# Kernel tuning notes

Measured on AMD Instinct MI355X. Metric: run time of the kernel, lower is better.

The kernel has to match this reference:

```python
import jax, jax.numpy as jnp
import numpy as np

N = 32768        # atoms
INV = 256        # irreps_in[inv_field].dim (scalar latent width)
MUL = 32         # input eq multiplicity: '32x1o'
VOUT = 4         # output eq multiplicity: '4x1o'
HID = 512        # ScalarMLPFunction latent dims [512, 512]
INV_OUT = 2      # inv_out_irreps '2x0e'
TYPES = 32       # num_types
EPS = 1e-10


def _mlp(x, w1, w2, w3):
    # ScalarMLPFunction: Linear(+1/sqrt(fan_in) norm) -> SiLU -> ... -> Linear
    h = jax.nn.silu((x @ w1) * (1.0 / np.sqrt(w1.shape[0])))
    h = jax.nn.silu((h @ w2) * (1.0 / np.sqrt(w2.shape[0])))
    return (h @ w3) * (1.0 / np.sqrt(w3.shape[0]))


def setup_inputs() -> dict:
    key = jax.random.key(0)
    ks = jax.random.split(key, 10)
    inv_features = jax.random.normal(ks[0], (N, INV), dtype=jnp.float32)
    eq_features = jax.random.normal(ks[1], (N, MUL, 3), dtype=jnp.float32)
    atom_types = jax.random.randint(ks[2], (N, 1), 0, TYPES, dtype=jnp.int32)
    # hypernetwork (final_latent): INV -> 512 -> 512 -> MUL*VOUT
    w1_lat = jax.random.normal(ks[3], (INV, HID), dtype=jnp.float32)
    w2_lat = jax.random.normal(ks[4], (HID, HID), dtype=jnp.float32)
    w3_lat = jax.random.normal(ks[5], (HID, MUL * VOUT), dtype=jnp.float32)
    # final_readout: INV -> 512 -> 512 -> INV_OUT
    w1_ro = jax.random.normal(ks[6], (INV, HID), dtype=jnp.float32)
    w2_ro = jax.random.normal(ks[7], (HID, HID), dtype=jnp.float32)
    w3_ro = jax.random.normal(ks[8], (HID, INV_OUT), dtype=jnp.float32)
    # atom_type2bond_lengths parameter, init to ones as in the module
    bond_lengths = jnp.ones((TYPES, VOUT, 1), dtype=jnp.float32)
    return dict(inv_features=inv_features, eq_features=eq_features,
                atom_types=atom_types, w1_lat=w1_lat, w2_lat=w2_lat,
                w3_lat=w3_lat, w1_ro=w1_ro, w2_ro=w2_ro, w3_ro=w3_ro,
                bond_lengths=bond_lengths)


def reference(inv_features, eq_features, atom_types, w1_lat, w2_lat, w3_lat,
              w1_ro, w2_ro, w3_ro, bond_lengths):
    # hypernet-generated per-atom weights for the equivariant Linear
    weights = _mlp(inv_features, w1_lat, w2_lat, w3_lat)          # [N, MUL*VOUT]
    weights = weights.reshape(-1, MUL, VOUT)                      # [N, u, v]
    inv_out = _mlp(inv_features, w1_ro, w2_ro, w3_ro)             # [N, INV_OUT]
    # e3nn Linear '32x1o -> 4x1o', shared_weights=False, path norm 1/sqrt(mul_in)
    eq = jnp.einsum('num,nuv->nvm', eq_features, weights) * (1.0 / np.sqrt(MUL))
    # norm -> divide -> nan_to_num
    norm = jnp.linalg.norm(eq, axis=-1, keepdims=True)            # [N, VOUT, 1]
    eq = jnp.nan_to_num(eq / (norm + EPS), nan=0.0)
    # per-atom-type bond-length scale (gather-multiply)
    eq = eq * bond_lengths[atom_types[:, 0]]                      # [N, VOUT, 3]
    return inv_out, eq
```

## Files before the change

kernel.cpp:

```cpp
#include <hip/hip_runtime.h>
#include <hip/hip_bf16.h>

#define N_ATOMS 32768

typedef __attribute__((ext_vector_type(4))) float f32x4;
typedef __attribute__((ext_vector_type(8))) short bf16x8;
typedef unsigned short u16;

__device__ __forceinline__ u16 f2b(float f) {
    union { __hip_bfloat16 b; u16 u; } c;
    c.b = __float2bfloat16(f);
    return c.u;
}
__device__ __forceinline__ float b2f(u16 u) {
    union { unsigned int i; float f; } c;
    c.i = ((unsigned int)u) << 16;
    return c.f;
}

#define GLDS16(src, dst) __builtin_amdgcn_global_load_lds( \
    (const __attribute__((address_space(1))) void*)(src),  \
    (__attribute__((address_space(3))) void*)(dst), 16, 0, 0)

__global__ void __launch_bounds__(256) setup_kernel(
        const float* __restrict__ x, u16* __restrict__ xhi, u16* __restrict__ xlo,
        const float* __restrict__ w1l, const float* __restrict__ w2l,
        const float* __restrict__ w3l, const float* __restrict__ w1r,
        const float* __restrict__ w2r,
        u16* __restrict__ W1LThi, u16* __restrict__ W1LTlo, u16* __restrict__ W1RT,
        u16* __restrict__ W2LThi, u16* __restrict__ W2LTlo, u16* __restrict__ W2RT,
        u16* __restrict__ W3LThi, u16* __restrict__ W3LTlo,
        float* __restrict__ out_inv) {
    int bid = blockIdx.x;
    if (bid < 4096) {
        size_t i = (size_t)(bid * 256 + threadIdx.x) * 8;
        float4 v0 = *(const float4*)(x + i);
        float4 v1 = *(const float4*)(x + i + 4);
        float v[8] = {v0.x, v0.y, v0.z, v0.w, v1.x, v1.y, v1.z, v1.w};
        bf16x8 rh, rl;
#pragma unroll
        for (int j = 0; j < 8; ++j) {
            u16 h = f2b(v[j]);
            rh[j] = (short)h;
            rl[j] = (short)f2b(v[j] - b2f(h));
        }
        *(bf16x8*)(xhi + i) = rh;
        *(bf16x8*)(xlo + i) = rl;
    } else if (bid < 7424) {
        int i = (bid - 4096) * 256 + threadIdx.x;
        if (i < 131072) {
            int n = i >> 8, k = i & 255;
            float v = w1l[k * 512 + n];
            u16 h = f2b(v);
            W1LThi[i] = h;
            W1LTlo[i] = f2b(v - b2f(h));
        } else if (i < 262144) {
            int j = i - 131072;
            int n = j >> 8, k = j & 255;
            W1RT[j] = f2b(w1r[k * 512 + n]);
        } else if (i < 524288) {
            int j = i - 262144;
            int n = j >> 9, k = j & 511;
            float v = w2l[k * 512 + n];
            u16 h = f2b(v);
            W2LThi[j] = h;
            W2LTlo[j] = f2b(v - b2f(h));
        } else if (i < 786432) {
            int j = i - 524288;
            int n = j >> 9, k = j & 511;
            W2RT[j] = f2b(w2r[k * 512 + n]);
        } else if (i < 851968) {
            int j = i - 786432;
            int n = j >> 9, k = j & 511;
            float v = w3l[k * 128 + n];
            u16 h = f2b(v);
            W3LThi[j] = h;
            W3LTlo[j] = f2b(v - b2f(h));
        }
    } else {
        int i = (bid - 7424) * 256 + threadIdx.x;
        *(float4*)(out_inv + i * 4) = float4{0.f, 0.f, 0.f, 0.f};
    }
}

template<int GX>
__global__ void __launch_bounds__(512, 1) gemm4p(
        const u16* __restrict__ Ahi, const u16* __restrict__ Alo,
        const u16* __restrict__ Bhi, const u16* __restrict__ Blo,
        u16* __restrict__ Chi, u16* __restrict__ Clo,
        int ldc, int K, float scale) {
    __shared__ __align__(16) u16 smem[65536];
    u16* const lA0 = smem;
    u16* const lB0 = smem + 32768;
    const int tid = threadIdx.x;
    const int lane = tid & 63;
    const int wid = tid >> 6;
    const int wm = wid >> 2;
    const int wn = wid & 3;
    const int rlane = lane & 15;
    const int kc = lane >> 4;
    const int srow0 = tid >> 2;
    const int scp = tid & 3;

    const int nwg = gridDim.x;
    const int bid = blockIdx.x;
    const int wg = (bid & 7) * (nwg >> 3) + (bid >> 3);
    const int bn = (wg % GX) * 256;
    const int bm = (wg / GX) * 256;

    const int kt = K >> 6;
    const int NT = 3 * kt;

    auto stageA = [&](int t, int buf, int kh) {
        int seg = (t >= kt) + (t >= 2 * kt);
        const u16* As = (seg == 1) ? Alo : Ahi;
        int k0 = (t - seg * kt) * 64 + kh * 32;
        u16* la = lA0 + buf * 16384 + kh * 8192;
#pragma unroll
        for (int call = 0; call < 2; ++call) {
            int row = call * 128 + srow0;
            int c = scp ^ ((row >> 1) & 3);
            GLDS16(As + (size_t)(bm + row) * K + k0 + c * 8, la + row * 32 + scp * 8);
        }
    };
    auto stageB = [&](int t, int buf, int kh) {
        int seg = (t >= kt) + (t >= 2 * kt);
        const u16* Bs = (seg == 2) ? Blo : Bhi;
        int k0 = (t - seg * kt) * 64 + kh * 32;
        u16* lb = lB0 + buf * 16384 + kh * 8192;
#pragma unroll
        for (int call = 0; call < 2; ++call) {
            int row = call * 128 + srow0;
            int c = scp ^ ((row >> 1) & 3);
            GLDS16(Bs + (size_t)(bn + row) * K + k0 + c * 8, lb + row * 32 + scp * 8);
        }
    };

    f32x4 acc[8][4] = {};
    bf16x8 af[4], bf[4];

#define RD_A(buf, kh, mh) do {                                                \
        const u16* la_ = lA0 + (buf) * 16384 + (kh) * 8192;                   \
        _Pragma("unroll")                                                     \
        for (int m_ = 0; m_ < 4; ++m_) {                                      \
            int row_ = wm * 128 + (mh) * 64 + m_ * 16 + rlane;                \
            int c_ = kc ^ ((row_ >> 1) & 3);                                  \
            af[m_] = *(const bf16x8*)&la_[row_ * 32 + c_ * 8];                \
        }                                                                     \
    } while (0)
#define RD_B(buf, kh) do {                                                    \
        const u16* lb_ = lB0 + (buf) * 16384 + (kh) * 8192;                   \
        _Pragma("unroll")                                                     \
        for (int n_ = 0; n_ < 4; ++n_) {                                      \
            int row_ = wn * 64 + n_ * 16 + rlane;                             \
            int c_ = kc ^ ((row_ >> 1) & 3);                                  \
            bf[n_] = *(const bf16x8*)&lb_[row_ * 32 + c_ * 8];                \
        }                                                                     \
    } while (0)
#define LGKM0 do {                                                            \
        asm volatile("s_waitcnt lgkmcnt(0)" ::: "memory");                    \
        __builtin_amdgcn_sched_barrier(0);                                    \
    } while (0)
#define MM(mh) do {                                                           \
        __builtin_amdgcn_s_setprio(1);                                        \
        _Pragma("unroll")                                                     \
        for (int m_ = 0; m_ < 4; ++m_)                                        \
            _Pragma("unroll")                                                 \
            for (int n_ = 0; n_ < 4; ++n_)                                    \
                acc[(mh) * 4 + m_][n_] = __builtin_amdgcn_mfma_f32_16x16x32_bf16( \
                    af[m_], bf[n_], acc[(mh) * 4 + m_][n_], 0, 0, 0);         \
        __builtin_amdgcn_s_setprio(0);                                        \
    } while (0)

    stageA(0, 0, 0);
    stageB(0, 0, 0);
    stageA(0, 0, 1);
    stageB(0, 0, 1);

    for (int t = 0; t < NT; ++t) {
        const int cur = t & 1, oth = cur ^ 1;
        const bool pf = (t + 1 < NT);
        asm volatile("s_waitcnt vmcnt(4)" ::: "memory");
        __builtin_amdgcn_s_barrier();
        RD_B(cur, 0);
        RD_A(cur, 0, 0);
        if (pf) stageA(t + 1, oth, 0);
        LGKM0;
        MM(0);
        RD_A(cur, 0, 1);
        if (pf) stageB(t + 1, oth, 0);
        LGKM0;
        MM(1);
        if (pf) asm volatile("s_waitcnt vmcnt(4)" ::: "memory");
        else    asm volatile("s_waitcnt vmcnt(0)" ::: "memory");
        __builtin_amdgcn_s_barrier();
        RD_B(cur, 1);
        RD_A(cur, 1, 0);
        if (pf) stageA(t + 1, oth, 1);
        LGKM0;
        MM(0);
        RD_A(cur, 1, 1);
        if (pf) stageB(t + 1, oth, 1);
        LGKM0;
        MM(1);
    }
#undef MM
#undef LGKM0
#undef RD_B
#undef RD_A

    const int g = lane >> 4;
#pragma unroll
    for (int m = 0; m < 8; ++m) {
        int grow0 = bm + wm * 128 + m * 16 + (g << 2);
#pragma unroll
        for (int n = 0; n < 4; ++n) {
            int gcol = bn + wn * 64 + n * 16 + rlane;
#pragma unroll
            for (int r = 0; r < 4; ++r) {
                float v = acc[m][n][r] * scale;
                v = v / (1.0f + __expf(-v));
                size_t idx = (size_t)(grow0 + r) * ldc + gcol;
                u16 h = f2b(v);
                Chi[idx] = h;
                Clo[idx] = f2b(v - b2f(h));
            }
        }
    }
}

template<int NSEG, int GX, int NF, bool SILU, int OUTK>
__global__ void __launch_bounds__(512, 2) gemm8p(
        const u16* __restrict__ Ahi, const u16* __restrict__ Alo,
        const u16* __restrict__ Bhi, const u16* __restrict__ Blo,
        void* __restrict__ Chi, void* __restrict__ Clo,
        int ldc, int K, float scale,
        const float* __restrict__ e_w3, float* __restrict__ e_out) {
    constexpr int LBSZ = NF * 64 * 64;
    constexpr int SMEMN = 32768 + 2 * LBSZ;
    __shared__ __align__(16) u16 smem[SMEMN];
    u16* const lA0 = smem;
    u16* const lB0 = smem + 32768;
    const int tid = threadIdx.x;
    const int lane = tid & 63;
    const int wid = tid >> 6;
    const int wm = wid >> 2;
    const int wn = wid & 3;
    const int rlane = lane & 15;
    const int kc = lane >> 4;
    const int cps = rlane & 7;
    const int srow = tid >> 3;
    const int scp = tid & 7;

    const int nwg = gridDim.x;
    const int bid = blockIdx.x;
    const int wg = (bid & 7) * (nwg >> 3) + (bid >> 3);
    const int bn = (wg % GX) * (NF * 64);
    const int bm = (wg / GX) * 256;

    const int kt = K >> 6;
    const int NT = NSEG * kt;

    auto stageA = [&](int t, int buf) {
        int seg = (NSEG == 1) ? 0 : ((t >= kt) + (t >= 2 * kt));
        const u16* As = (NSEG == 1) ? Ahi : (seg == 1 ? Alo : Ahi);
        int k0 = (t - seg * kt) << 6;
        u16* la = lA0 + buf * 16384;
#pragma unroll
        for (int call = 0; call < 4; ++call) {
            int row = call * 64 + srow;
            int c = scp ^ (row & 7);
            GLDS16(As + (size_t)(bm + row) * K + k0 + c * 8, la + (size_t)(row * 64 + scp * 8));
        }
    };
    auto stageB = [&](int t, int buf) {
        int seg = (NSEG == 1) ? 0 : ((t >= kt) + (t >= 2 * kt));
        const u16* Bs = (NSEG == 1) ? Bhi : (seg == 2 ? Blo : Bhi);
        int k0 = (t - seg * kt) << 6;
        u16* lb = lB0 + buf * LBSZ;
#pragma unroll
        for (int call = 0; call < NF; ++call) {
            int row = call * 64 + srow;
            int c = scp ^ (row & 7);
            GLDS16(Bs + (size_t)(bn + row) * K + k0 + c * 8, lb + (size_t)(row * 64 + scp * 8));
        }
    };

    f32x4 acc[8][NF] = {};

    stageA(0, 0);
    stageB(0, 0);
    asm volatile("s_waitcnt vmcnt(0)" ::: "memory");
    __builtin_amdgcn_s_barrier();

    for (int t = 0; t < NT; ++t) {
        const int cur = t & 1, nxt = cur ^ 1;
        const bool pf = (t + 1 < NT);
        const u16* la = lA0 + cur * 16384;
        const u16* lb = lB0 + cur * LBSZ;
#pragma unroll
        for (int ks = 0; ks < 2; ++ks) {
            bf16x8 af[8], bfr[NF];
            const int cp = (ks * 4 + kc) ^ cps;
#pragma unroll
            for (int m = 0; m < 8; ++m) {
                int row = wm * 128 + m * 16 + rlane;
                af[m] = *(const bf16x8*)&la[row * 64 + cp * 8];
            }
#pragma unroll
            for (int n = 0; n < NF; ++n) {
                int row = wn * (NF * 16) + n * 16 + rlane;
                bfr[n] = *(const bf16x8*)&lb[row * 64 + cp * 8];
            }
            if (pf) {
                if (ks == 0) stageA(t + 1, nxt);
                else         stageB(t + 1, nxt);
            }
            asm volatile("s_waitcnt lgkmcnt(0)" ::: "memory");
            __builtin_amdgcn_sched_barrier(0);
            __builtin_amdgcn_s_setprio(1);
#pragma unroll
            for (int m = 0; m < 8; ++m)
#pragma unroll
                for (int n = 0; n < NF; ++n)
                    acc[m][n] = __builtin_amdgcn_mfma_f32_16x16x32_bf16(af[m], bfr[n], acc[m][n], 0, 0, 0);
            __builtin_amdgcn_s_setprio(0);
        }
        asm volatile("s_waitcnt vmcnt(0)" ::: "memory");
        __builtin_amdgcn_s_barrier();
    }

    const int g = lane >> 4;

    if constexpr (OUTK == 3) {
        const float s512f = 0.04419417382415922f;
        float wj0[NF], wj1[NF];
#pragma unroll
        for (int n = 0; n < NF; ++n) {
            int gc = bn + wn * (NF * 16) + n * 16 + rlane;
            wj0[n] = e_w3[gc * 2] * s512f;
            wj1[n] = e_w3[gc * 2 + 1] * s512f;
        }
#pragma unroll
        for (int m = 0; m < 8; ++m)
#pragma unroll
            for (int r = 0; r < 4; ++r) {
                float s0 = 0.f, s1 = 0.f;
#pragma unroll
                for (int n = 0; n < NF; ++n) {
                    float v = acc[m][n][r] * scale;
                    v = v / (1.0f + __expf(-v));
                    s0 = fmaf(v, wj0[n], s0);
                    s1 = fmaf(v, wj1[n], s1);
                }
#pragma unroll
                for (int off = 1; off < 16; off <<= 1) {
                    s0 += __shfl_xor(s0, off);
                    s1 += __shfl_xor(s1, off);
                }
                if (rlane == 0) {
                    int row = bm + wm * 128 + m * 16 + g * 4 + r;
                    atomicAdd(&e_out[row * 2], s0);
                    atomicAdd(&e_out[row * 2 + 1], s1);
                }
            }
    } else {
#pragma unroll
        for (int m = 0; m < 8; ++m) {
            int grow0 = bm + wm * 128 + m * 16 + (g << 2);
#pragma unroll
            for (int n = 0; n < NF; ++n) {
                int gcol = bn + wn * (NF * 16) + n * 16 + rlane;
#pragma unroll
                for (int r = 0; r < 4; ++r) {
                    float v = acc[m][n][r] * scale;
                    if constexpr (SILU) v = v / (1.0f + __expf(-v));
                    size_t idx = (size_t)(grow0 + r) * ldc + gcol;
                    if constexpr (OUTK == 0) ((float*)Chi)[idx] = v;
                    else                     ((u16*)Chi)[idx] = f2b(v);
                }
            }
        }
    }
}

__global__ void eq_kernel(const float* __restrict__ eqf, const float* __restrict__ wgt,
                          const int* __restrict__ types, const float* __restrict__ bond,
                          float* __restrict__ out) {
    int t = blockIdx.x * 256 + threadIdx.x;
    int n = t >> 2, v = t & 3;
    const float* e = eqf + (size_t)n * 96;
    const float* w = wgt + (size_t)n * 128 + v;
    float a0 = 0.f, a1 = 0.f, a2 = 0.f;
#pragma unroll
    for (int u = 0; u < 32; ++u) {
        float wv = w[u * 4];
        a0 = fmaf(e[u * 3 + 0], wv, a0);
        a1 = fmaf(e[u * 3 + 1], wv, a1);
        a2 = fmaf(e[u * 3 + 2], wv, a2);
    }
    const float s = 0.17677669529663687f;
    a0 *= s; a1 *= s; a2 *= s;
    float norm = sqrtf(a0 * a0 + a1 * a1 + a2 * a2) + 1e-10f;
    float bl = bond[types[n] * 4 + v];
    float r0 = a0 / norm, r1 = a1 / norm, r2 = a2 / norm;
    if (isnan(r0)) r0 = 0.f;
    if (isnan(r1)) r1 = 0.f;
    if (isnan(r2)) r2 = 0.f;
    out[(size_t)n * 12 + v * 3 + 0] = r0 * bl;
    out[(size_t)n * 12 + v * 3 + 1] = r1 * bl;
    out[(size_t)n * 12 + v * 3 + 2] = r2 * bl;
}

extern "C" void kernel_launch(void* const* d_in, const int* in_sizes, int n_in,
                              void* d_out, int out_size, void* d_ws, size_t ws_size,
                              hipStream_t stream) {
    const float* inv  = (const float*)d_in[0];
    const float* eqf  = (const float*)d_in[1];
    const int*   typs = (const int*)d_in[2];
    const float* w1l  = (const float*)d_in[3];
    const float* w2l  = (const float*)d_in[4];
    const float* w3l  = (const float*)d_in[5];
    const float* w1r  = (const float*)d_in[6];
    const float* w2r  = (const float*)d_in[7];
    const float* w3r  = (const float*)d_in[8];
    const float* bond = (const float*)d_in[9];

    char* ws = (char*)d_ws;
    const size_t MB = 1024 * 1024, KB = 1024;
    u16* XHI   = (u16*)(ws);
    u16* XLO   = (u16*)(ws + 16 * MB);
    u16* H1R   = (u16*)(ws + 32 * MB);
    u16* H1Lhi = (u16*)(ws + 64 * MB);
    u16* H1Llo = (u16*)(ws + 96 * MB);
    u16* H2Lhi = (u16*)(ws);
    u16* H2Llo = (u16*)(ws + 128 * MB);
    float* WGT = (float*)(ws + 32 * MB);
    char* wb = ws + 160 * MB;
    u16* W1LThi = (u16*)(wb);
    u16* W1LTlo = (u16*)(wb + 256 * KB);
    u16* W1RT   = (u16*)(wb + 512 * KB);
    u16* W2LThi = (u16*)(wb + 768 * KB);
    u16* W2LTlo = (u16*)(wb + 1280 * KB);
    u16* W2RT   = (u16*)(wb + 1792 * KB);
    u16* W3LThi = (u16*)(wb + 2304 * KB);
    u16* W3LTlo = (u16*)(wb + 2432 * KB);

    float* out_inv = (float*)d_out;
    float* out_eq  = (float*)d_out + N_ATOMS * 2;

    const float s256 = 0.0625f;
    const float s512 = 0.04419417382415922f;

    setup_kernel<<<dim3(7488), dim3(256), 0, stream>>>(
        inv, XHI, XLO, w1l, w2l, w3l, w1r, w2r,
        W1LThi, W1LTlo, W1RT, W2LThi, W2LTlo, W2RT, W3LThi, W3LTlo, out_inv);
    gemm4p<2><<<dim3(256), dim3(512), 0, stream>>>(
        XHI, XLO, W1LThi, W1LTlo, H1Lhi, H1Llo, 512, 256, s256);
    gemm8p<1, 2, 4, true, 1><<<dim3(256), dim3(512), 0, stream>>>(
        XHI, nullptr, W1RT, nullptr, H1R, nullptr, 512, 256, s256, nullptr, nullptr);
    gemm8p<1, 2, 4, true, 3><<<dim3(256), dim3(512), 0, stream>>>(
        H1R, nullptr, W2RT, nullptr, nullptr, nullptr, 0, 512, s512, w3r, out_inv);
    gemm4p<2><<<dim3(256), dim3(512), 0, stream>>>(
        H1Lhi, H1Llo, W2LThi, W2LTlo, H2Lhi, H2Llo, 512, 512, s512);
    gemm8p<3, 2, 1, false, 0><<<dim3(256), dim3(512), 0, stream>>>(
        H2Lhi, H2Llo, W3LThi, W3LTlo, WGT, nullptr, 128, 512, s512, nullptr, nullptr);
    eq_kernel<<<dim3(512), dim3(256), 0, stream>>>(eqf, WGT, typs, bond, out_eq);
}
```

Before: 196.4 us.

## Restructure split-bf16 GEMM into 8-wave ping-pong with 64-wide K tiles

Replaces the 4-phase gemm4p with gemm8x, used for the first two latent MLP layers. The LDS layout changes from two 32-wide K halves per tile to row-halves with 64-wide K rows and an 8-way XOR swizzle. The main loop becomes a barrier-separated ping-pong schedule where each wave group alternates MFMA bursts with LDS reads and global-to-LDS prefetch. The aim is better overlap of MFMA with memory traffic and fewer LDS bank conflicts, at the cost of many more barriers and a full vmcnt(0) drain every iteration.

```diff
diff --git a/kernel.cpp b/kernel.cpp
--- a/kernel.cpp
+++ b/kernel.cpp
@@ -84,23 +84,24 @@
 }
 
 template<int GX>
-__global__ void __launch_bounds__(512, 1) gemm4p(
+__global__ void __launch_bounds__(512, 1) gemm8x(
         const u16* __restrict__ Ahi, const u16* __restrict__ Alo,
         const u16* __restrict__ Bhi, const u16* __restrict__ Blo,
         u16* __restrict__ Chi, u16* __restrict__ Clo,
         int ldc, int K, float scale) {
     __shared__ __align__(16) u16 smem[65536];
-    u16* const lA0 = smem;
-    u16* const lB0 = smem + 32768;
     const int tid = threadIdx.x;
     const int lane = tid & 63;
     const int wid = tid >> 6;
     const int wm = wid >> 2;
     const int wn = wid & 3;
+    const int bh = wn >> 1;
+    const int br0 = (wn & 1) * 64;
     const int rlane = lane & 15;
     const int kc = lane >> 4;
-    const int srow0 = tid >> 2;
-    const int scp = tid & 3;
+    const int cps = rlane & 7;
+    const int srow = tid >> 3;
+    const int scp = tid & 7;
 
     const int nwg = gridDim.x;
     const int bid = blockIdx.x;
@@ -111,103 +112,81 @@
     const int kt = K >> 6;
     const int NT = 3 * kt;
 
-    auto stageA = [&](int t, int buf, int kh) {
+    auto stage = [&](int t, int mat, int h) {
         int seg = (t >= kt) + (t >= 2 * kt);
-        const u16* As = (seg == 1) ? Alo : Ahi;
-        int k0 = (t - seg * kt) * 64 + kh * 32;
-        u16* la = lA0 + buf * 16384 + kh * 8192;
+        int k0 = (t - seg * kt) << 6;
+        int buf = t & 1;
+        const u16* src = (mat == 0) ? ((seg == 1) ? Alo : Ahi)
+                                    : ((seg == 2) ? Blo : Bhi);
+        int grow = ((mat == 0) ? bm : bn) + h * 128;
+        u16* dst = smem + mat * 32768 + buf * 16384 + h * 8192;
 #pragma unroll
         for (int call = 0; call < 2; ++call) {
-            int row = call * 128 + srow0;
-            int c = scp ^ ((row >> 1) & 3);
-            GLDS16(As + (size_t)(bm + row) * K + k0 + c * 8, la + row * 32 + scp * 8);
-        }
-    };
-    auto stageB = [&](int t, int buf, int kh) {
-        int seg = (t >= kt) + (t >= 2 * kt);
-        const u16* Bs = (seg == 2) ? Blo : Bhi;
-        int k0 = (t - seg * kt) * 64 + kh * 32;
-        u16* lb = lB0 + buf * 16384 + kh * 8192;
-#pragma unroll
-        for (int call = 0; call < 2; ++call) {
-            int row = call * 128 + srow0;
-            int c = scp ^ ((row >> 1) & 3);
-            GLDS16(Bs + (size_t)(bn + row) * K + k0 + c * 8, lb + row * 32 + scp * 8);
+            int row = call * 64 + srow;
+            int c = scp ^ (row & 7);
+            GLDS16(src + (size_t)(grow + row) * K + k0 + c * 8, dst + row * 64 + scp * 8);
         }
     };
 
     f32x4 acc[8][4] = {};
     bf16x8 af[4], bf[4];
 
-#define RD_A(buf, kh, mh) do {                                                \
-        const u16* la_ = lA0 + (buf) * 16384 + (kh) * 8192;                   \
-        _Pragma("unroll")                                                     \
-        for (int m_ = 0; m_ < 4; ++m_) {                                      \
-            int row_ = wm * 128 + (mh) * 64 + m_ * 16 + rlane;                \
-            int c_ = kc ^ ((row_ >> 1) & 3);                                  \
-            af[m_] = *(const bf16x8*)&la_[row_ * 32 + c_ * 8];                \
-        }                                                                     \
+#define RD_B(buf, kk) do {                                                     \
+        const u16* lb_ = smem + 32768 + (buf) * 16384 + bh * 8192;             \
+        _Pragma("unroll")                                                      \
+        for (int n_ = 0; n_ < 4; ++n_) {                                       \
+            int row_ = br0 + n_ * 16 + rlane;                                  \
+            bf[n_] = *(const bf16x8*)&lb_[row_ * 64 + (((kk) * 4 + kc) ^ cps) * 8]; \
+        }                                                                      \
     } while (0)
-#define RD_B(buf, kh) do {                                                    \
-        const u16* lb_ = lB0 + (buf) * 16384 + (kh) * 8192;                   \
-        _Pragma("unroll")                                                     \
-        for (int n_ = 0; n_ < 4; ++n_) {                                      \
-            int row_ = wn * 64 + n_ * 16 + rlane;                             \
-            int c_ = kc ^ ((row_ >> 1) & 3);                                  \
-            bf[n_] = *(const bf16x8*)&lb_[row_ * 32 + c_ * 8];                \
-        }                                                                     \
+#define RD_A(buf, mh, kk) do {                                                 \
+        const u16* la_ = smem + (buf) * 16384 + wm * 8192;                     \
+        _Pragma("unroll")                                                      \
+        for (int m_ = 0; m_ < 4; ++m_) {                                       \
+            int row_ = (mh) * 64 + m_ * 16 + rlane;                            \
+            af[m_] = *(const bf16x8*)&la_[row_ * 64 + (((kk) * 4 + kc) ^ cps) * 8]; \
+        }                                                                      \
     } while (0)
-#define LGKM0 do {                                                            \
-        asm volatile("s_waitcnt lgkmcnt(0)" ::: "memory");                    \
-        __builtin_amdgcn_sched_barrier(0);                                    \
+#define MM(mh) do {                                                            \
+        asm volatile("s_waitcnt lgkmcnt(0)" ::: "memory");                     \
+        __builtin_amdgcn_sched_barrier(0);                                     \
+        __builtin_amdgcn_s_setprio(1);                                         \
+        _Pragma("unroll")                                                      \
+        for (int m_ = 0; m_ < 4; ++m_)                                         \
+            _Pragma("unroll")                                                  \
+            for (int n_ = 0; n_ < 4; ++n_)                                     \
+                acc[(mh) * 4 + m_][n_] = __builtin_amdgcn_mfma_f32_16x16x32_bf16( \
+                    af[m_], bf[n_], acc[(mh) * 4 + m_][n_], 0, 0, 0);          \
+        __builtin_amdgcn_s_setprio(0);                                         \
     } while (0)
-#define MM(mh) do {                                                           \
-        __builtin_amdgcn_s_setprio(1);                                        \
-        _Pragma("unroll")                                                     \
-        for (int m_ = 0; m_ < 4; ++m_)                                        \
-            _Pragma("unroll")                                                 \
-            for (int n_ = 0; n_ < 4; ++n_)                                    \
-                acc[(mh) * 4 + m_][n_] = __builtin_amdgcn_mfma_f32_16x16x32_bf16( \
-                    af[m_], bf[n_], acc[(mh) * 4 + m_][n_], 0, 0, 0);         \
-        __builtin_amdgcn_s_setprio(0);                                        \
-    } while (0)
-
-    stageA(0, 0, 0);
-    stageB(0, 0, 0);
-    stageA(0, 0, 1);
-    stageB(0, 0, 1);
+#define BAR __builtin_amdgcn_s_barrier()
+
+    stage(0, 0, 0); stage(0, 0, 1); stage(0, 1, 0); stage(0, 1, 1);
+    asm volatile("s_waitcnt vmcnt(0)" ::: "memory");
+    BAR;
 
     for (int t = 0; t < NT; ++t) {
-        const int cur = t & 1, oth = cur ^ 1;
+        const int buf = t & 1;
         const bool pf = (t + 1 < NT);
-        asm volatile("s_waitcnt vmcnt(4)" ::: "memory");
-        __builtin_amdgcn_s_barrier();
-        RD_B(cur, 0);
-        RD_A(cur, 0, 0);
-        if (pf) stageA(t + 1, oth, 0);
-        LGKM0;
-        MM(0);
-        RD_A(cur, 0, 1);
-        if (pf) stageB(t + 1, oth, 0);
-        LGKM0;
-        MM(1);
-        if (pf) asm volatile("s_waitcnt vmcnt(4)" ::: "memory");
-        else    asm volatile("s_waitcnt vmcnt(0)" ::: "memory");
-        __builtin_amdgcn_s_barrier();
-        RD_B(cur, 1);
-        RD_A(cur, 1, 0);
-        if (pf) stageA(t + 1, oth, 1);
-        LGKM0;
-        MM(0);
-        RD_A(cur, 1, 1);
-        if (pf) stageB(t + 1, oth, 1);
-        LGKM0;
-        MM(1);
-    }
+        RD_B(buf, 0); RD_A(buf, 0, 0);
+        if (pf) stage(t + 1, 0, 0);
+        BAR; MM(0); BAR;
+        RD_A(buf, 1, 0);
+        if (pf) stage(t + 1, 0, 1);
+        BAR; MM(1); BAR;
+        RD_B(buf, 1); RD_A(buf, 0, 1);
+        if (pf) stage(t + 1, 1, 0);
+        BAR; MM(0); BAR;
+        RD_A(buf, 1, 1);
+        if (pf) stage(t + 1, 1, 1);
+        BAR; MM(1);
+        asm volatile("s_waitcnt vmcnt(0)" ::: "memory");
+        BAR;
+    }
+#undef BAR
 #undef MM
-#undef LGKM0
+#undef RD_A
 #undef RD_B
-#undef RD_A
 
     const int g = lane >> 4;
 #pragma unroll
@@ -455,13 +434,13 @@
     setup_kernel<<<dim3(7488), dim3(256), 0, stream>>>(
         inv, XHI, XLO, w1l, w2l, w3l, w1r, w2r,
         W1LThi, W1LTlo, W1RT, W2LThi, W2LTlo, W2RT, W3LThi, W3LTlo, out_inv);
-    gemm4p<2><<<dim3(256), dim3(512), 0, stream>>>(
+    gemm8x<2><<<dim3(256), dim3(512), 0, stream>>>(
         XHI, XLO, W1LThi, W1LTlo, H1Lhi, H1Llo, 512, 256, s256);
     gemm8p<1, 2, 4, true, 1><<<dim3(256), dim3(512), 0, stream>>>(
         XHI, nullptr, W1RT, nullptr, H1R, nullptr, 512, 256, s256, nullptr, nullptr);
     gemm8p<1, 2, 4, true, 3><<<dim3(256), dim3(512), 0, stream>>>(
         H1R, nullptr, W2RT, nullptr, nullptr, nullptr, 0, 512, s512, w3r, out_inv);
-    gemm4p<2><<<dim3(256), dim3(512), 0, stream>>>(
+    gemm8x<2><<<dim3(256), dim3(512), 0, stream>>>(
         H1Lhi, H1Llo, W2LThi, W2LTlo, H2Lhi, H2Llo, 512, 512, s512);
     gemm8p<3, 2, 1, false, 0><<<dim3(256), dim3(512), 0, stream>>>(
         H2Lhi, H2Llo, W3LThi, W3LTlo, WGT, nullptr, 128, 512, s512, nullptr, nullptr);
```

After: 206.4 us. 1.05x slower.
